# Kernel tuning notes

Hardware: AMD Instinct MI355X
Metric: run time of the kernel (lower is better)

Reference implementation:

```python
import jax, jax.numpy as jnp
import numpy as np

B, M, PAST, FUT, NPRED, D = 512, 32768, 8, 12, 20, 48


def _gru_step(h, x, w_ih, w_hh, b_ih, b_hh):
    # torch GRU cell: gates ordered [r, z, n]
    gi = x @ w_ih.T + b_ih
    gh = h @ w_hh.T + b_hh
    ir, iz, inn = jnp.split(gi, 3, axis=-1)
    hr, hz, hn = jnp.split(gh, 3, axis=-1)
    r = jax.nn.sigmoid(ir + hr)
    z = jax.nn.sigmoid(iz + hz)
    n = jnp.tanh(inn + r * hn)
    return (1.0 - z) * n + z * h


def setup_inputs() -> dict:
    key = jax.random.key(0)
    ks = jax.random.split(key, 16)
    f32 = jnp.float32
    def rn(k, shp, sc):
        return (jax.random.normal(k, shp, dtype=f32) * sc)
    return {
        "past": jax.random.normal(ks[0], (B, PAST, 2), dtype=f32),
        "obs_traj": jax.random.normal(ks[1], (B, PAST, 2), dtype=f32),
        "conv_w": rn(ks[2], (D, 2, 3), 0.3),
        "conv_b": jnp.zeros((D,), f32),
        "enc_w_ih": rn(ks[3], (3 * D, D), 0.1),
        "enc_w_hh": rn(ks[4], (3 * D, D), 0.1),
        "enc_b_ih": jnp.zeros((3 * D,), f32),
        "enc_b_hh": jnp.zeros((3 * D,), f32),
        "memory_past": jax.random.normal(ks[5], (M, D), dtype=f32),
        "memory_fut": jax.random.normal(ks[6], (M, D), dtype=f32),
        "Wq": rn(ks[7], (D, D), 0.1), "bq": jnp.zeros((D,), f32),
        "Wk": rn(ks[8], (D, D), 0.1), "bk": jnp.zeros((D,), f32),
        "Wv": rn(ks[9], (D, D), 0.1), "bv": jnp.zeros((D,), f32),
        "dec_w_ih": rn(ks[10], (6 * D, 2 * D), 0.1),
        "dec_w_hh": rn(ks[11], (6 * D, 2 * D), 0.1),
        "dec_b_ih": jnp.zeros((6 * D,), f32),
        "dec_b_hh": jnp.zeros((6 * D,), f32),
        "fc_w": rn(ks[12], (2, 2 * D), 0.1),
        "fc_b": jnp.zeros((2,), f32),
    }


def reference(past, obs_traj, conv_w, conv_b, enc_w_ih, enc_w_hh, enc_b_ih, enc_b_hh,
              memory_past, memory_fut, Wq, bq, Wk, bk, Wv, bv,
              dec_w_ih, dec_w_hh, dec_b_ih, dec_b_hh, fc_w, fc_b):
    b = past.shape[0]
    # --- past encoder: Conv1d(2,48,3,pad=1) + ReLU, then GRU(48,48) ---
    x = jnp.transpose(past, (0, 2, 1))                     # [B,2,T]
    emb = jax.lax.conv_general_dilated(
        x, conv_w, (1,), [(1, 1)], dimension_numbers=("NCH", "OIH", "NCH"))
    emb = jax.nn.relu(emb + conv_b[None, :, None])         # [B,48,T]
    emb = jnp.transpose(emb, (2, 0, 1))                    # [T,B,48] for scan

    def enc_step(h, x_t):
        return _gru_step(h, x_t, enc_w_ih, enc_w_hh, enc_b_ih, enc_b_hh), None
    state_past, _ = jax.lax.scan(enc_step, jnp.zeros((b, D), past.dtype), emb)  # [B,48]

    # --- iterative refinement: 20 rounds of attention over the full memory ---
    # Lin_K/Lin_V are applied to the same (full) banks every iteration -> hoist.
    K = memory_past @ Wk.T + bk                            # [M,48]
    V = memory_fut @ Wv.T + bv                             # [M,48]

    def irm_step(c, _):
        q = c @ Wq.T + bq                                  # [B,48]
        a = jax.nn.softmax(q @ K.T, axis=-1)               # [B,M], scale=1.0
        att = a @ V                                        # [B,48]
        return q + att, att
    _, atts = jax.lax.scan(irm_step, state_past, None, length=NPRED)  # [20,B,48]
    pred = jnp.transpose(atts, (1, 0, 2)).reshape(-1, D)   # [B*20,48] (b-major)

    # --- GRU(96,96) decoder, future_len steps, input only at t=0 ---
    n = b * NPRED
    present = jnp.repeat(obs_traj[:, -1], NPRED, axis=0)   # [B*20,2]
    sp = jnp.repeat(state_past, NPRED, axis=0)             # [B*20,48]
    info = jnp.concatenate([sp, pred], axis=1)             # [B*20,96]
    xs = jnp.concatenate(
        [info[None], jnp.zeros((FUT - 1, n, 2 * D), info.dtype)], axis=0)

    def dec_step(carry, x_t):
        h, pres = carry
        h = _gru_step(h, x_t, dec_w_ih, dec_w_hh, dec_b_ih, dec_b_hh)
        pres = pres + (h @ fc_w.T + fc_b)
        return (h, pres), pres
    _, coords = jax.lax.scan(
        dec_step, (jnp.zeros((n, 2 * D), info.dtype), present), xs)  # [FUT,B*20,2]

    prediction = jnp.transpose(coords, (1, 0, 2)).reshape(b, NPRED, FUT, 2)
    return prediction
```

## Files before the change

### kernel.cpp

```cpp
#include <hip/hip_runtime.h>

typedef unsigned short u16;
typedef unsigned int u32;
typedef __attribute__((ext_vector_type(8))) short short8v;
typedef __attribute__((ext_vector_type(4))) float f32x4;

#define GLD_LDS(g, l) __builtin_amdgcn_global_load_lds( \
    (const __attribute__((address_space(1))) void*)(g), \
    (__attribute__((address_space(3))) void*)(l), 16, 0, 0)

#define LOG2E 1.44269504f

__device__ __forceinline__ u16 f2bf(float f){
  union { float f; u32 u; } v; v.f = f;
  u32 r = v.u + 0x7FFFu + ((v.u >> 16) & 1u);
  return (u16)(r >> 16);
}
__device__ __forceinline__ float bf2f(u16 h){
  union { u32 u; float f; } v; v.u = ((u32)h) << 16;
  return v.f;
}
__device__ __forceinline__ u32 pk2(float a, float b){
  union { float f; u32 u; } x, y; x.f = a; y.f = b;
  return __builtin_amdgcn_perm(y.u + 0x8000u, x.u + 0x8000u, 0x07060302u);
}
__device__ __forceinline__ float sigm(float x){ return 1.f/(1.f+__expf(-x)); }
__device__ __forceinline__ float tanh_fast(float x){ return 1.f - 2.f/(1.f+__expf(2.f*x)); }

__global__ void prep_kernel(const float* dih, const float* dhh,
    const float* eih, const float* ehh, const float* wq, const float* wk, const float* wv,
    u16* Dih, u16* Dhh, u16* Eih, u16* Ehh, u16* Qf, u16* Kf, u16* Vf)
{
  int idx = blockIdx.x*256 + threadIdx.x;
  const float* src; u16* dst; int KC, Kc, e;
  if      (idx < 27648){ src=dih; dst=Dih; KC=3; Kc=96; e=idx; }
  else if (idx < 55296){ src=dhh; dst=Dhh; KC=3; Kc=96; e=idx-27648; }
  else if (idx < 64512){ src=eih; dst=Eih; KC=2; Kc=48; e=idx-55296; }
  else if (idx < 73728){ src=ehh; dst=Ehh; KC=2; Kc=48; e=idx-64512; }
  else if (idx < 76800){ src=wq;  dst=Qf;  KC=2; Kc=48; e=idx-73728; }
  else if (idx < 79872){ src=wk;  dst=Kf;  KC=2; Kc=48; e=idx-76800; }
  else if (idx < 82944){ src=wv;  dst=Vf;  KC=2; Kc=48; e=idx-79872; }
  else return;
  int j = e & 7, ln = (e>>3) & 15, qd = (e>>7) & 3, tkc = e>>9;
  int kc = tkc % KC, nt = tkc / KC;
  int g = nt*16 + ln, k = kc*32 + qd*8 + j;
  dst[e] = (k < Kc) ? f2bf(src[g*Kc + k]) : (u16)0;
}

__global__ __launch_bounds__(256) void setup_kernel(
    const float* past, const float* conv_w, const float* conv_b,
    const float* enc_b_ih, const float* enc_b_hh,
    const float* memory_past, const float* memory_fut,
    const float* bq, const float* bk, const float* bv,
    const u16* EihF, const u16* EhhF, const u16* WqF, const u16* WkF, const u16* WvF,
    float* stateP, float* qf, u16* qbB, u16* Kb, u16* Vc)
{
  __shared__ __align__(16) char SMEM[61440];
  const int tid = threadIdx.x, bx = blockIdx.x;
  const int wid = tid>>6, lane = tid&63, qd = lane>>4, ln = lane&15;
  f32x4 zf = {0.f,0.f,0.f,0.f};

  if (bx >= 504){
    int eb = bx - 504;
    u16* sWih = (u16*)(SMEM);
    u16* sWhh = (u16*)(SMEM + 18432);
    u16* sWq  = (u16*)(SMEM + 36864);
    float* sCw = (float*)(SMEM + 43008);
    float* sCb = (float*)(SMEM + 44160);
    float* sPast = (float*)(SMEM + 44352);
    u16* sHbW = (u16*)(SMEM + 48448 + wid*2304);
    for (int i = wid; i < 18; i += 4) GLD_LDS((const char*)EihF + i*1024 + lane*16, SMEM + i*1024);
    for (int i = wid; i < 18; i += 4) GLD_LDS((const char*)EhhF + i*1024 + lane*16, SMEM + 18432 + i*1024);
    for (int i = wid; i < 6;  i += 4) GLD_LDS((const char*)WqF  + i*1024 + lane*16, SMEM + 36864 + i*1024);
    for (int i = tid; i < 288; i += 256) sCw[i] = conv_w[i];
    if (tid < 48) sCb[tid] = conv_b[tid];
    for (int i = tid; i < 1024; i += 256) sPast[i] = past[eb*1024 + i];
    __syncthreads();
    short8v aE[8][2];
    {
      const float* pr = &sPast[(wid*16 + ln)*16];
      for (int t = 0; t < 8; ++t)
        for (int kc = 0; kc < 2; ++kc){
          union { short8v v; u16 h[8]; } u;
          #pragma unroll
          for (int j = 0; j < 8; ++j){
            int d = kc*32 + qd*8 + j;
            float a = 0.f;
            if (d < 48){
              a = sCb[d];
              #pragma unroll
              for (int kt = 0; kt < 3; ++kt){
                int tau = t + kt - 1;
                if (tau >= 0 && tau < 8){
                  a += pr[tau*2+0]*sCw[d*6+kt];
                  a += pr[tau*2+1]*sCw[d*6+3+kt];
                }
              }
              a = fmaxf(a, 0.f);
            }
            u.h[j] = (d < 48) ? f2bf(a) : (u16)0;
          }
          aE[t][kc] = u.v;
        }
    }
    for (int i = lane; i < 576; i += 64) ((u32*)sHbW)[i] = 0;
    float biR[3],biZ[3],biN[3],bhR[3],bhZ[3],bhN[3];
    #pragma unroll
    for (int i = 0; i < 3; ++i){
      int d = i*16 + ln;
      biR[i]=enc_b_ih[d]; biZ[i]=enc_b_ih[48+d]; biN[i]=enc_b_ih[96+d];
      bhR[i]=enc_b_hh[d]; bhZ[i]=enc_b_hh[48+d]; bhN[i]=enc_b_hh[96+d];
    }
    float hreg[3][4];
    #pragma unroll
    for (int i=0;i<3;++i) for (int r=0;r<4;++r) hreg[i][r]=0.f;
    int r0 = eb*64 + wid*16;
    #pragma unroll 1
    for (int t = 0; t < 8; ++t){
      short8v aH0 = *(const short8v*)&sHbW[ln*72 + qd*8];
      short8v aH1 = *(const short8v*)&sHbW[ln*72 + 32 + qd*8];
      f32x4 gI[9], gH[9];
      #pragma unroll
      for (int nt = 0; nt < 9; ++nt){ gI[nt] = zf; gH[nt] = zf; }
      #pragma unroll
      for (int nt = 0; nt < 9; ++nt){
        gI[nt] = __builtin_amdgcn_mfma_f32_16x16x32_bf16(aE[t][0], *(const short8v*)&sWih[((nt*2+0)*4+qd)*128 + ln*8], gI[nt], 0,0,0);
        gI[nt] = __builtin_amdgcn_mfma_f32_16x16x32_bf16(aE[t][1], *(const short8v*)&sWih[((nt*2+1)*4+qd)*128 + ln*8], gI[nt], 0,0,0);
        gH[nt] = __builtin_amdgcn_mfma_f32_16x16x32_bf16(aH0, *(const short8v*)&sWhh[((nt*2+0)*4+qd)*128 + ln*8], gH[nt], 0,0,0);
        gH[nt] = __builtin_amdgcn_mfma_f32_16x16x32_bf16(aH1, *(const short8v*)&sWhh[((nt*2+1)*4+qd)*128 + ln*8], gH[nt], 0,0,0);
      }
      #pragma unroll
      for (int i3 = 0; i3 < 3; ++i3)
        #pragma unroll
        for (int r = 0; r < 4; ++r){
          float rr = sigm(gI[i3][r]+biR[i3] + gH[i3][r]+bhR[i3]);
          float zz = sigm(gI[i3+3][r]+biZ[i3] + gH[i3+3][r]+bhZ[i3]);
          float nn = tanh_fast(gI[i3+6][r]+biN[i3] + rr*(gH[i3+6][r]+bhN[i3]));
          float hv = (1.f-zz)*nn + zz*hreg[i3][r];
          hreg[i3][r] = hv;
          sHbW[(qd*4+r)*72 + i3*16 + ln] = f2bf(hv);
        }
    }
    #pragma unroll
    for (int i3 = 0; i3 < 3; ++i3)
      #pragma unroll
      for (int r = 0; r < 4; ++r)
        stateP[(r0+qd*4+r)*48 + i3*16 + ln] = hreg[i3][r];
    short8v aH0 = *(const short8v*)&sHbW[ln*72 + qd*8];
    short8v aH1 = *(const short8v*)&sHbW[ln*72 + 32 + qd*8];
    f32x4 q3[3];
    #pragma unroll
    for (int nt = 0; nt < 3; ++nt){
      q3[nt] = zf;
      q3[nt] = __builtin_amdgcn_mfma_f32_16x16x32_bf16(aH0, *(const short8v*)&sWq[((nt*2+0)*4+qd)*128 + ln*8], q3[nt], 0,0,0);
      q3[nt] = __builtin_amdgcn_mfma_f32_16x16x32_bf16(aH1, *(const short8v*)&sWq[((nt*2+1)*4+qd)*128 + ln*8], q3[nt], 0,0,0);
    }
    #pragma unroll
    for (int nt = 0; nt < 3; ++nt)
      #pragma unroll
      for (int r = 0; r < 4; ++r){
        int row = r0 + qd*4 + r, d = nt*16 + ln;
        float v = q3[nt][r] + bq[d];
        qf[row*48 + d] = v;
        qbB[row*64 + d] = f2bf(v * LOG2E);
      }
    #pragma unroll
    for (int r = 0; r < 4; ++r)
      if (ln < 8) *(u32*)&qbB[(r0+qd*4+r)*64 + 48 + ln*2] = 0;
  } else {
    u16* sWkF = (u16*)(SMEM);
    u16* sWvF = (u16*)(SMEM + 6144);
    u16* smp  = (u16*)(SMEM + 12288 + wid*2304);
    u16* smf  = (u16*)(SMEM + 21504 + wid*2304);
    u16* sKT  = (u16*)(SMEM + 30720);
    u16* sVT  = (u16*)(SMEM + 38912);
    for (int i = wid; i < 6; i += 4) GLD_LDS((const char*)WkF + i*1024 + lane*16, SMEM + i*1024);
    for (int i = wid; i < 6; i += 4) GLD_LDS((const char*)WvF + i*1024 + lane*16, SMEM + 6144 + i*1024);
    float bkv[3], bvv[3];
    #pragma unroll
    for (int nt = 0; nt < 3; ++nt){ bkv[nt] = bk[nt*16+ln]; bvv[nt] = bv[nt*16+ln]; }
    int ntile = (bx < 8) ? 2 : 1;
    for (int tt = 0; tt < ntile; ++tt){
      int tile = (tt == 0) ? bx : (504 + bx);
      int r0 = tile*64 + wid*16;
      for (int i = lane; i < 576; i += 64){ ((u32*)smp)[i] = 0; ((u32*)smf)[i] = 0; }
      for (int i = lane; i < 768; i += 64){
        int r = i/48, c = i - r*48;
        smp[r*72+c] = f2bf(memory_past[(size_t)r0*48 + i]);
        smf[r*72+c] = f2bf(memory_fut[(size_t)r0*48 + i]);
      }
      __syncthreads();
      short8v aP0 = *(const short8v*)&smp[ln*72 + qd*8];
      short8v aP1 = *(const short8v*)&smp[ln*72 + 32 + qd*8];
      short8v aF0 = *(const short8v*)&smf[ln*72 + qd*8];
      short8v aF1 = *(const short8v*)&smf[ln*72 + 32 + qd*8];
      f32x4 k3[3], v3[3];
      #pragma unroll
      for (int nt = 0; nt < 3; ++nt){ k3[nt] = zf; v3[nt] = zf; }
      #pragma unroll
      for (int nt = 0; nt < 3; ++nt){
        k3[nt] = __builtin_amdgcn_mfma_f32_16x16x32_bf16(aP0, *(const short8v*)&sWkF[((nt*2+0)*4+qd)*128 + ln*8], k3[nt], 0,0,0);
        k3[nt] = __builtin_amdgcn_mfma_f32_16x16x32_bf16(aP1, *(const short8v*)&sWkF[((nt*2+1)*4+qd)*128 + ln*8], k3[nt], 0,0,0);
        v3[nt] = __builtin_amdgcn_mfma_f32_16x16x32_bf16(aF0, *(const short8v*)&sWvF[((nt*2+0)*4+qd)*128 + ln*8], v3[nt], 0,0,0);
        v3[nt] = __builtin_amdgcn_mfma_f32_16x16x32_bf16(aF1, *(const short8v*)&sWvF[((nt*2+1)*4+qd)*128 + ln*8], v3[nt], 0,0,0);
      }
      for (int i = lane; i < 128; i += 64) ((u32*)sKT)[(wid*16 + (i>>3))*32 + 24 + (i&7)] = 0;
      #pragma unroll
      for (int nt = 0; nt < 3; ++nt)
        #pragma unroll
        for (int r = 0; r < 4; ++r){
          int keyl = wid*16 + qd*4 + r, d = nt*16 + ln;
          sKT[keyl*64 + d] = f2bf(k3[nt][r] + bkv[nt]);
          sVT[d*72 + keyl] = f2bf(v3[nt][r] + bvv[nt]);
        }
      __syncthreads();
      for (int i = tid; i < 512; i += 256)
        *(uint4*)((char*)(Kb + (size_t)tile*64*64) + i*16) = *(const uint4*)((char*)sKT + i*16);
      for (int i = tid; i < 384; i += 256){
        int d = i>>3, sub = i&7;
        *(uint4*)((char*)(Vc + ((size_t)((tile*64)>>8)*48 + d)*256 + ((tile*64)&255)) + sub*16)
            = *(const uint4*)((char*)sVT + d*144 + sub*16);
      }
      __syncthreads();
    }
  }
}

__global__ __launch_bounds__(256, 1) void iter_kernel(int mode, int it,
    const u16* qbB, const u16* Kb, const u16* Vc, const u16* WqF, const float* bq,
    const float* qfP, float* qfC, float* pred,
    const float* mP, const float* lP, const float* aP,
    float* mC, float* lC, float* aC)
{
  __shared__ __align__(16) char SMEM[55936];
  u16*   sQ  = (u16*)(SMEM + 45056);
  float* sWc = (float*)(SMEM + 49152);
  float* sLg = (float*)(SMEM + 51200);
  u16*   sCb = (u16*)(SMEM + 51332);
  const int tid = threadIdx.x, bx = blockIdx.x;
  const int wid = tid>>6, lane = tid&63, qd = lane>>4, ln = lane&15;
  const int rg = bx>>4, ch = bx&15;
  const int rowbase = rg*32;
  f32x4 zf = {0.f,0.f,0.f,0.f};

  if (mode == 1){
    float* sRed = (float*)SMEM;
    {
      int row = tid>>3, jj = tid&7, grow = rowbase + row;
      float m0 = mP[grow*16 + jj*2], m1 = mP[grow*16 + jj*2+1];
      float l0 = lP[grow*16 + jj*2], l1 = lP[grow*16 + jj*2+1];
      float mg = fmaxf(m0, m1);
      #pragma unroll
      for (int k = 1; k < 8; k <<= 1) mg = fmaxf(mg, __shfl_xor(mg, k));
      float w0 = exp2f(m0 - mg), w1 = exp2f(m1 - mg);
      float wl = w0*l0 + w1*l1;
      #pragma unroll
      for (int k = 1; k < 8; k <<= 1) wl += __shfl_xor(wl, k);
      sWc[row*16 + jj*2] = w0; sWc[row*16 + jj*2+1] = w1;
      if (jj == 0) sLg[row] = wl;
    }
    __syncthreads();
    {
      f32x4 accv[6];
      #pragma unroll
      for (int i = 0; i < 6; ++i) accv[i] = zf;
      #pragma unroll
      for (int ci = 0; ci < 4; ++ci){
        int c = wid*4 + ci;
        const f32x4* slab = (const f32x4*)(aP + ((size_t)c*512 + rowbase)*48);
        #pragma unroll
        for (int i = 0; i < 6; ++i){
          f32x4 v = slab[i*64 + lane];
          int rr = (i*64 + lane)/12;
          float w = sWc[rr*16 + c];
          accv[i][0] += w*v[0]; accv[i][1] += w*v[1];
          accv[i][2] += w*v[2]; accv[i][3] += w*v[3];
        }
      }
      float* red = sRed + wid*1536;
      #pragma unroll
      for (int i = 0; i < 6; ++i)
        *(f32x4*)&red[(i*64 + lane)*4] = accv[i];
    }
    __syncthreads();
    {
      int row = tid>>3, jj = tid&7, grow = rowbase + row;
      float lg = sLg[row];
      int base = row*48 + jj*6;
      #pragma unroll
      for (int d6 = 0; d6 < 6; ++d6){
        int d = jj*6 + d6;
        float s = sRed[base+d6] + sRed[1536+base+d6] + sRed[3072+base+d6] + sRed[4608+base+d6];
        float a = s / lg;
        if (ch == 0) pred[(size_t)(grow*20 + (it-1))*48 + d] = a;
        sCb[row*72 + d] = f2bf(qfP[grow*48 + d] + a);
      }
      ((u32*)&sCb[row*72 + 48])[jj] = 0;
    }
    __syncthreads();
    if (wid < 2){
      short8v ac0 = *(const short8v*)&sCb[(wid*16+ln)*72 + qd*8];
      short8v ac1 = *(const short8v*)&sCb[(wid*16+ln)*72 + 32 + qd*8];
      f32x4 q3[3];
      #pragma unroll
      for (int nt = 0; nt < 3; ++nt){
        q3[nt] = zf;
        q3[nt] = __builtin_amdgcn_mfma_f32_16x16x32_bf16(ac0, *(const short8v*)&WqF[((nt*2+0)*4+qd)*128 + ln*8], q3[nt], 0,0,0);
        q3[nt] = __builtin_amdgcn_mfma_f32_16x16x32_bf16(ac1, *(const short8v*)&WqF[((nt*2+1)*4+qd)*128 + ln*8], q3[nt], 0,0,0);
      }
      #pragma unroll
      for (int nt = 0; nt < 3; ++nt)
        #pragma unroll
        for (int r = 0; r < 4; ++r){
          int lr = wid*16 + qd*4 + r, d = nt*16 + ln;
          float v = q3[nt][r] + bq[d];
          if (ch == 0) qfC[(rowbase + lr)*48 + d] = v;
          sQ[lr*64 + d] = f2bf(v * LOG2E);
        }
    } else {
      for (int i = tid-128; i < 256; i += 128){
        int r2 = i>>3, p = i&7;
        ((u32*)&sQ[r2*64 + 48])[p] = 0;
      }
    }
    __syncthreads();
  } else {
    const u32* src = (const u32*)(qbB + rowbase*64);
    ((u32*)sQ)[tid]       = src[tid];
    ((u32*)sQ)[256 + tid] = src[256 + tid];
    ((u32*)sQ)[512 + tid] = src[512 + tid];
    ((u32*)sQ)[768 + tid] = src[768 + tid];
    __syncthreads();
  }

  const int wslice = ch*2048 + wid*512;
  u16* sp8 = (u16*)(SMEM + 26624);
  short8v aq[2][2];
  #pragma unroll
  for (int rt = 0; rt < 2; ++rt)
    #pragma unroll
    for (int kc = 0; kc < 2; ++kc)
      aq[rt][kc] = *(const short8v*)&sQ[(rt*16+ln)*64 + kc*32 + qd*8];
  f32x4 acc[2][3];
  #pragma unroll
  for (int rt = 0; rt < 2; ++rt) for (int dt = 0; dt < 3; ++dt) acc[rt][dt] = zf;
  float mrun[2] = {-3.0e38f, -3.0e38f}, lrun[2] = {0.f, 0.f};
  u16* spb[2] = { sp8 + (wid*2+0)*1152, sp8 + (wid*2+1)*1152 };

  #pragma unroll
  for (int kt = 0; kt < 8; ++kt){
    const int tb = wslice + kt*64;
    const u16* kb = Kb + (size_t)tb*64;
    const u16* vb = Vc + (size_t)(tb>>8)*48*256 + (tb & 255);
    short8v kf[4][2], vf[2][3];
    #pragma unroll
    for (int nt = 0; nt < 4; ++nt)
      #pragma unroll
      for (int kc = 0; kc < 2; ++kc)
        kf[nt][kc] = *(const short8v*)&kb[(nt*16+ln)*64 + kc*32 + qd*8];
    #pragma unroll
    for (int kc = 0; kc < 2; ++kc)
      #pragma unroll
      for (int dt = 0; dt < 3; ++dt)
        vf[kc][dt] = *(const short8v*)&vb[(dt*16+ln)*256 + kc*32 + qd*8];
    f32x4 s[2][4];
    #pragma unroll
    for (int rt = 0; rt < 2; ++rt)
      #pragma unroll
      for (int nt = 0; nt < 4; ++nt){
        f32x4 z = zf;
        z = __builtin_amdgcn_mfma_f32_16x16x32_bf16(kf[nt][0], aq[rt][0], z, 0,0,0);
        z = __builtin_amdgcn_mfma_f32_16x16x32_bf16(kf[nt][1], aq[rt][1], z, 0,0,0);
        s[rt][nt] = z;
      }
    #pragma unroll
    for (int rt = 0; rt < 2; ++rt){
      float vmax = fmaxf(fmaxf(fmaxf(s[rt][0][0], s[rt][0][1]), fmaxf(s[rt][0][2], s[rt][0][3])),
                   fmaxf(fmaxf(s[rt][1][0], s[rt][1][1]), fmaxf(s[rt][1][2], s[rt][1][3])));
      vmax = fmaxf(vmax, fmaxf(fmaxf(fmaxf(s[rt][2][0], s[rt][2][1]), fmaxf(s[rt][2][2], s[rt][2][3])),
                   fmaxf(fmaxf(s[rt][3][0], s[rt][3][1]), fmaxf(s[rt][3][2], s[rt][3][3]))));
      vmax = fmaxf(vmax, __shfl_xor(vmax, 16));
      vmax = fmaxf(vmax, __shfl_xor(vmax, 32));
      float mnew = fmaxf(mrun[rt], vmax);
      float alpha = exp2f(mrun[rt] - mnew);
      mrun[rt] = mnew;
      u16* sp = spb[rt];
      float lsum = 0.f;
      #pragma unroll
      for (int nt = 0; nt < 4; ++nt){
        float p0 = exp2f(s[rt][nt][0]-mnew), p1 = exp2f(s[rt][nt][1]-mnew);
        float p2 = exp2f(s[rt][nt][2]-mnew), p3 = exp2f(s[rt][nt][3]-mnew);
        lsum += (p0+p1)+(p2+p3);
        uint2 pk; pk.x = pk2(p0,p1); pk.y = pk2(p2,p3);
        *(uint2*)&sp[ln*72 + nt*16 + qd*4] = pk;
      }
      lsum += __shfl_xor(lsum, 16);
      lsum += __shfl_xor(lsum, 32);
      lrun[rt] = lrun[rt]*alpha + lsum;
      #pragma unroll
      for (int dt = 0; dt < 3; ++dt){
        acc[rt][dt][0] *= alpha; acc[rt][dt][1] *= alpha;
        acc[rt][dt][2] *= alpha; acc[rt][dt][3] *= alpha;
      }
      short8v pb0 = *(const short8v*)&sp[ln*72 + qd*8];
      short8v pb1 = *(const short8v*)&sp[ln*72 + 32 + qd*8];
      #pragma unroll
      for (int dt = 0; dt < 3; ++dt){
        acc[rt][dt] = __builtin_amdgcn_mfma_f32_16x16x32_bf16(vf[0][dt], pb0, acc[rt][dt], 0,0,0);
        acc[rt][dt] = __builtin_amdgcn_mfma_f32_16x16x32_bf16(vf[1][dt], pb1, acc[rt][dt], 0,0,0);
      }
    }
  }
  __syncthreads();
  float* sMg = (float*)SMEM;
  #pragma unroll
  for (int rt = 0; rt < 2; ++rt)
    #pragma unroll
    for (int dt = 0; dt < 3; ++dt)
      #pragma unroll
      for (int r = 0; r < 4; ++r)
        sMg[wid*1600 + (rt*16+ln)*50 + dt*16 + qd*4 + r] = acc[rt][dt][r];
  if (lane < 16){
    sMg[wid*1600 + ln*50 + 48] = mrun[0]; sMg[wid*1600 + ln*50 + 49] = lrun[0];
    sMg[wid*1600 + (16+ln)*50 + 48] = mrun[1]; sMg[wid*1600 + (16+ln)*50 + 49] = lrun[1];
  }
  __syncthreads();
  {
    int row = tid>>3, jj = tid&7, grow = rowbase + row;
    float m0 = sMg[row*50+48], m1 = sMg[1600+row*50+48];
    float m2 = sMg[3200+row*50+48], m3 = sMg[4800+row*50+48];
    float mg = fmaxf(fmaxf(m0,m1), fmaxf(m2,m3));
    float e0 = exp2f(m0-mg), e1 = exp2f(m1-mg), e2 = exp2f(m2-mg), e3 = exp2f(m3-mg);
    float lg = e0*sMg[row*50+49] + e1*sMg[1600+row*50+49]
             + e2*sMg[3200+row*50+49] + e3*sMg[4800+row*50+49];
    if (jj == 0){ mC[grow*16 + ch] = mg; lC[grow*16 + ch] = lg; }
    int d0 = jj*6;
    #pragma unroll
    for (int d6 = 0; d6 < 6; ++d6){
      int d = d0 + d6;
      aC[((size_t)ch*512 + grow)*48 + d] =
          e0*sMg[row*50+d] + e1*sMg[1600+row*50+d]
        + e2*sMg[3200+row*50+d] + e3*sMg[4800+row*50+d];
    }
  }
}

__global__ __launch_bounds__(384, 1) void dec_kernel(
    const u16* Dihf, const u16* Dhhf, const float* b_ih, const float* b_hh,
    const float* stateP, const float* pred, const float* obs,
    const float* mF, const float* lF, const float* aF,
    const float* fc_w, const float* fc_b, float* out)
{
  __shared__ __align__(16) u16 sx[2][16*106];
  __shared__ float sPx[2][6][16], sPy[2][6][16];
  const int tid = threadIdx.x, bx = blockIdx.x;
  const int wid = tid>>6, lane = tid&63, qd = lane>>4, ln = lane&15;
  const int rw = bx*16;
  f32x4 zf = {0.f,0.f,0.f,0.f};

  for (int i = tid; i < 1536; i += 384){
    int r = i/96, k = i - r*96;
    int row = rw + r, b20 = row/20;
    float v = (k < 48) ? stateP[b20*48 + k] : pred[(size_t)row*48 + (k-48)];
    sx[0][r*106 + k] = f2bf(v);
  }
  if (tid < 48){
    int r19 = (19 - (rw % 20)) % 20;
    if (r19 < 16){
      int b = (rw + r19)/20;
      float mg = -3.0e38f, mv[16];
      #pragma unroll
      for (int c = 0; c < 16; ++c){ mv[c] = mF[b*16 + c]; mg = fmaxf(mg, mv[c]); }
      float num = 0.f, den = 0.f;
      #pragma unroll
      for (int c = 0; c < 16; ++c){
        float w = exp2f(mv[c] - mg);
        den += w * lF[b*16 + c];
        num += w * aF[((size_t)c*512 + b)*48 + tid];
      }
      sx[0][r19*106 + 48 + tid] = f2bf(num/den);
    }
  }
  short8v whh[3][3];
  #pragma unroll
  for (int g = 0; g < 3; ++g)
    #pragma unroll
    for (int kc = 0; kc < 3; ++kc)
      whh[g][kc] = *(const short8v*)&Dhhf[(((g*6+wid)*3+kc)*4+qd)*128 + ln*8];
  const int d = wid*16 + ln;
  float biR=b_ih[d], biZ=b_ih[96+d], biN=b_ih[192+d];
  float bhR=b_hh[d], bhZ=b_hh[96+d], bhN=b_hh[192+d];
  float fw0=fc_w[d], fw1=fc_w[96+d];
  float hold[4] = {0.f,0.f,0.f,0.f};
  float fcb0 = fc_b[0], fcb1 = fc_b[1];
  float pres0 = 0.f, pres1 = 0.f;
  if (wid == 0 && lane < 16){
    int b20 = (rw + lane)/20;
    pres0 = obs[b20*16 + 14];
    pres1 = obs[b20*16 + 15];
  }
  __syncthreads();

  #pragma unroll 1
  for (int t = 0; t < 12; ++t){
    const u16* sr = sx[t&1];
    u16* sw = sx[(t+1)&1];
    short8v xa0 = *(const short8v*)&sr[ln*106 + qd*8];
    short8v xa1 = *(const short8v*)&sr[ln*106 + 32 + qd*8];
    short8v xa2 = *(const short8v*)&sr[ln*106 + 64 + qd*8];
    f32x4 acc[3] = {zf, zf, zf};
    if (t == 0){
      #pragma unroll
      for (int g = 0; g < 3; ++g){
        int nt = g*6 + wid;
        acc[g] = __builtin_amdgcn_mfma_f32_16x16x32_bf16(xa0, *(const short8v*)&Dihf[((nt*3+0)*4+qd)*128 + ln*8], acc[g], 0,0,0);
        acc[g] = __builtin_amdgcn_mfma_f32_16x16x32_bf16(xa1, *(const short8v*)&Dihf[((nt*3+1)*4+qd)*128 + ln*8], acc[g], 0,0,0);
        acc[g] = __builtin_amdgcn_mfma_f32_16x16x32_bf16(xa2, *(const short8v*)&Dihf[((nt*3+2)*4+qd)*128 + ln*8], acc[g], 0,0,0);
      }
    } else {
      #pragma unroll
      for (int g = 0; g < 3; ++g){
        acc[g] = __builtin_amdgcn_mfma_f32_16x16x32_bf16(xa0, whh[g][0], acc[g], 0,0,0);
        acc[g] = __builtin_amdgcn_mfma_f32_16x16x32_bf16(xa1, whh[g][1], acc[g], 0,0,0);
        acc[g] = __builtin_amdgcn_mfma_f32_16x16x32_bf16(xa2, whh[g][2], acc[g], 0,0,0);
      }
    }
    float px[4], py[4];
    #pragma unroll
    for (int r = 0; r < 4; ++r){
      float rr = sigm(acc[0][r] + biR + bhR);
      float zz = sigm(acc[1][r] + biZ + bhZ);
      float nn = (t == 0) ? tanh_fast(acc[2][r] + biN + rr*bhN)
                          : tanh_fast(biN + rr*(acc[2][r] + bhN));
      float hv = (1.f-zz)*nn + zz*hold[r];
      hold[r] = hv;
      sw[(qd*4+r)*106 + d] = f2bf(hv);
      px[r] = fw0*hv;
      py[r] = fw1*hv;
    }
    #pragma unroll
    for (int msk = 8; msk >= 1; msk >>= 1)
      #pragma unroll
      for (int r = 0; r < 4; ++r){
        px[r] += __shfl_xor(px[r], msk);
        py[r] += __shfl_xor(py[r], msk);
      }
    if (ln == 0){
      #pragma unroll
      for (int r = 0; r < 4; ++r){
        sPx[t&1][wid][qd*4+r] = px[r];
        sPy[t&1][wid][qd*4+r] = py[r];
      }
    }
    __syncthreads();
    if (wid == 0 && lane < 16){
      float fx = 0.f, fy = 0.f;
      #pragma unroll
      for (int w = 0; w < 6; ++w){ fx += sPx[t&1][w][lane]; fy += sPy[t&1][w][lane]; }
      pres0 += fx + fcb0;
      pres1 += fy + fcb1;
      out[((size_t)(rw + lane)*12 + t)*2 + 0] = pres0;
      out[((size_t)(rw + lane)*12 + t)*2 + 1] = pres1;
    }
  }
}

extern "C" void kernel_launch(void* const* d_in, const int* in_sizes, int n_in,
                              void* d_out, int out_size, void* d_ws, size_t ws_size,
                              hipStream_t stream)
{
  const float* past        = (const float*)d_in[0];
  const float* obs         = (const float*)d_in[1];
  const float* conv_w      = (const float*)d_in[2];
  const float* conv_b      = (const float*)d_in[3];
  const float* enc_w_ih    = (const float*)d_in[4];
  const float* enc_w_hh    = (const float*)d_in[5];
  const float* enc_b_ih    = (const float*)d_in[6];
  const float* enc_b_hh    = (const float*)d_in[7];
  const float* memory_past = (const float*)d_in[8];
  const float* memory_fut  = (const float*)d_in[9];
  const float* Wq = (const float*)d_in[10];
  const float* bq = (const float*)d_in[11];
  const float* Wk = (const float*)d_in[12];
  const float* bk = (const float*)d_in[13];
  const float* Wv = (const float*)d_in[14];
  const float* bv = (const float*)d_in[15];
  const float* dec_w_ih = (const float*)d_in[16];
  const float* dec_w_hh = (const float*)d_in[17];
  const float* dec_b_ih = (const float*)d_in[18];
  const float* dec_b_hh = (const float*)d_in[19];
  const float* fc_w = (const float*)d_in[20];
  const float* fc_b = (const float*)d_in[21];
  float* out = (float*)d_out;

  char* ws = (char*)d_ws;
  size_t off = 0;
  auto alloc = [&](size_t bytes){ void* p = ws + off; off += (bytes + 255) & ~(size_t)255; return p; };
  float* stateP = (float*)alloc(512*48*4);
  float* qfA    = (float*)alloc(512*48*4);
  float* qfB    = (float*)alloc(512*48*4);
  u16*   qbB    = (u16*)alloc(512*64*2);
  float* mB[2], *lB[2], *aB[2];
  for (int i = 0; i < 2; ++i){
    mB[i] = (float*)alloc(512*16*4);
    lB[i] = (float*)alloc(512*16*4);
    aB[i] = (float*)alloc((size_t)512*16*48*4);
  }
  float* pred = (float*)alloc((size_t)10240*48*4);
  u16*   Kb   = (u16*)alloc((size_t)32768*64*2);
  u16*   Vc   = (u16*)alloc((size_t)32768*48*2);
  u16*   Dihf = (u16*)alloc(27648*2);
  u16*   Dhhf = (u16*)alloc(27648*2);
  u16*   EihF = (u16*)alloc(9216*2);
  u16*   EhhF = (u16*)alloc(9216*2);
  u16*   WqF  = (u16*)alloc(3072*2);
  u16*   WkF  = (u16*)alloc(3072*2);
  u16*   WvF  = (u16*)alloc(3072*2);
  float* qbuf[2] = { qfA, qfB };

  prep_kernel<<<324, 256, 0, stream>>>(dec_w_ih, dec_w_hh, enc_w_ih, enc_w_hh,
                                       Wq, Wk, Wv, Dihf, Dhhf, EihF, EhhF, WqF, WkF, WvF);

  setup_kernel<<<512, 256, 0, stream>>>(
      past, conv_w, conv_b, enc_b_ih, enc_b_hh, memory_past, memory_fut,
      bq, bk, bv, EihF, EhhF, WqF, WkF, WvF,
      stateP, qfA, qbB, Kb, Vc);

  iter_kernel<<<256, 256, 0, stream>>>(0, 0, qbB, Kb, Vc, WqF, bq,
      qfA, qfA, pred, mB[1], lB[1], aB[1], mB[0], lB[0], aB[0]);
  for (int it = 1; it < 20; ++it){
    int pv = (it-1)&1, cu = it&1;
    iter_kernel<<<256, 256, 0, stream>>>(1, it, qbB, Kb, Vc, WqF, bq,
        qbuf[pv], qbuf[cu], pred, mB[pv], lB[pv], aB[pv], mB[cu], lB[cu], aB[cu]);
  }

  dec_kernel<<<640, 384, 0, stream>>>(Dihf, Dhhf, dec_b_ih, dec_b_hh,
      stateP, pred, obs, mB[1], lB[1], aB[1], fc_w, fc_b, out);
}
```

Baseline: 628.7 us.

## Spread encoder GRU over more blocks, store partial attention in bf16, tweak decoder stride

Result: faster. 584.2 us (-7.1%).

```diff
diff --git a/kernel.cpp b/kernel.cpp
--- a/kernel.cpp
+++ b/kernel.cpp
@@ -19,6 +19,12 @@
 __device__ __forceinline__ float bf2f(u16 h){
   union { u32 u; float f; } v; v.u = ((u32)h) << 16;
   return v.f;
+}
+__device__ __forceinline__ float bflo(u32 x){
+  union { u32 u; float f; } v; v.u = x << 16; return v.f;
+}
+__device__ __forceinline__ float bfhi(u32 x){
+  union { u32 u; float f; } v; v.u = x & 0xFFFF0000u; return v.f;
 }
 __device__ __forceinline__ u32 pk2(float a, float b){
   union { float f; u32 u; } x, y; x.f = a; y.f = b;
@@ -60,26 +66,29 @@
   const int wid = tid>>6, lane = tid&63, qd = lane>>4, ln = lane&15;
   f32x4 zf = {0.f,0.f,0.f,0.f};
 
-  if (bx >= 504){
-    int eb = bx - 504;
-    u16* sWih = (u16*)(SMEM);
-    u16* sWhh = (u16*)(SMEM + 18432);
-    u16* sWq  = (u16*)(SMEM + 36864);
-    float* sCw = (float*)(SMEM + 43008);
-    float* sCb = (float*)(SMEM + 44160);
-    float* sPast = (float*)(SMEM + 44352);
-    u16* sHbW = (u16*)(SMEM + 48448 + wid*2304);
-    for (int i = wid; i < 18; i += 4) GLD_LDS((const char*)EihF + i*1024 + lane*16, SMEM + i*1024);
-    for (int i = wid; i < 18; i += 4) GLD_LDS((const char*)EhhF + i*1024 + lane*16, SMEM + 18432 + i*1024);
-    for (int i = wid; i < 6;  i += 4) GLD_LDS((const char*)WqF  + i*1024 + lane*16, SMEM + 36864 + i*1024);
+  if (bx >= 480){
+    const int eb = bx - 480;
+    const int r0 = eb*16;
+    u16*   sWf  = (u16*)(SMEM);
+    u16*   gIb  = (u16*)(SMEM + 18432);
+    u16*   sHb0 = (u16*)(SMEM + 55296);
+    u16*   sHb1 = (u16*)(SMEM + 57600);
+    float* sCw  = (float*)(SMEM + 57600);
+    float* sCb  = (float*)(SMEM + 58752);
+    float* sPast= (float*)(SMEM + 58944);
+
+    for (int i = wid; i < 18; i += 4) GLD_LDS((const char*)EihF + i*1024 + lane*16, (char*)sWf + i*1024);
     for (int i = tid; i < 288; i += 256) sCw[i] = conv_w[i];
     if (tid < 48) sCb[tid] = conv_b[tid];
-    for (int i = tid; i < 1024; i += 256) sPast[i] = past[eb*1024 + i];
-    __syncthreads();
-    short8v aE[8][2];
-    {
-      const float* pr = &sPast[(wid*16 + ln)*16];
-      for (int t = 0; t < 8; ++t)
+    for (int i = tid; i < 256; i += 256) sPast[i] = past[r0*16 + i];
+    __syncthreads();
+    #pragma unroll
+    for (int tt = 0; tt < 2; ++tt){
+      int t = wid*2 + tt;
+      short8v aE[2];
+      {
+        const float* pr = &sPast[ln*16];
+        #pragma unroll
         for (int kc = 0; kc < 2; ++kc){
           union { short8v v; u16 h[8]; } u;
           #pragma unroll
@@ -100,73 +109,93 @@
             }
             u.h[j] = (d < 48) ? f2bf(a) : (u16)0;
           }
-          aE[t][kc] = u.v;
+          aE[kc] = u.v;
         }
-    }
-    for (int i = lane; i < 576; i += 64) ((u32*)sHbW)[i] = 0;
-    float biR[3],biZ[3],biN[3],bhR[3],bhZ[3],bhN[3];
-    #pragma unroll
-    for (int i = 0; i < 3; ++i){
-      int d = i*16 + ln;
-      biR[i]=enc_b_ih[d]; biZ[i]=enc_b_ih[48+d]; biN[i]=enc_b_ih[96+d];
-      bhR[i]=enc_b_hh[d]; bhZ[i]=enc_b_hh[48+d]; bhN[i]=enc_b_hh[96+d];
-    }
-    float hreg[3][4];
-    #pragma unroll
-    for (int i=0;i<3;++i) for (int r=0;r<4;++r) hreg[i][r]=0.f;
-    int r0 = eb*64 + wid*16;
+      }
+      f32x4 gI[9];
+      #pragma unroll
+      for (int nt = 0; nt < 9; ++nt) gI[nt] = zf;
+      #pragma unroll
+      for (int nt = 0; nt < 9; ++nt){
+        gI[nt] = __builtin_amdgcn_mfma_f32_16x16x32_bf16(aE[0], *(const short8v*)&sWf[((nt*2+0)*4+qd)*128 + ln*8], gI[nt], 0,0,0);
+        gI[nt] = __builtin_amdgcn_mfma_f32_16x16x32_bf16(aE[1], *(const short8v*)&sWf[((nt*2+1)*4+qd)*128 + ln*8], gI[nt], 0,0,0);
+      }
+      #pragma unroll
+      for (int nt = 0; nt < 9; ++nt)
+        #pragma unroll
+        for (int r = 0; r < 4; ++r)
+          gIb[t*2304 + (qd*4+r)*144 + nt*16 + ln] = f2bf(gI[nt][r]);
+    }
+    __syncthreads();
+    for (int i = wid; i < 18; i += 4) GLD_LDS((const char*)EhhF + i*1024 + lane*16, (char*)sWf + i*1024);
+    for (int i = tid; i < 1152; i += 256) ((u32*)sHb0)[i] = 0;
+    __syncthreads();
+
+    const int g = wid;
+    float biR=0, biZ=0, biN=0, bhR=0, bhZ=0, bhN=0;
+    if (g < 3){
+      int d = g*16 + ln;
+      biR = enc_b_ih[d]; biZ = enc_b_ih[48+d]; biN = enc_b_ih[96+d];
+      bhR = enc_b_hh[d]; bhZ = enc_b_hh[48+d]; bhN = enc_b_hh[96+d];
+    }
+    float hold[4] = {0.f,0.f,0.f,0.f};
     #pragma unroll 1
     for (int t = 0; t < 8; ++t){
-      short8v aH0 = *(const short8v*)&sHbW[ln*72 + qd*8];
-      short8v aH1 = *(const short8v*)&sHbW[ln*72 + 32 + qd*8];
-      f32x4 gI[9], gH[9];
-      #pragma unroll
-      for (int nt = 0; nt < 9; ++nt){ gI[nt] = zf; gH[nt] = zf; }
-      #pragma unroll
-      for (int nt = 0; nt < 9; ++nt){
-        gI[nt] = __builtin_amdgcn_mfma_f32_16x16x32_bf16(aE[t][0], *(const short8v*)&sWih[((nt*2+0)*4+qd)*128 + ln*8], gI[nt], 0,0,0);
-        gI[nt] = __builtin_amdgcn_mfma_f32_16x16x32_bf16(aE[t][1], *(const short8v*)&sWih[((nt*2+1)*4+qd)*128 + ln*8], gI[nt], 0,0,0);
-        gH[nt] = __builtin_amdgcn_mfma_f32_16x16x32_bf16(aH0, *(const short8v*)&sWhh[((nt*2+0)*4+qd)*128 + ln*8], gH[nt], 0,0,0);
-        gH[nt] = __builtin_amdgcn_mfma_f32_16x16x32_bf16(aH1, *(const short8v*)&sWhh[((nt*2+1)*4+qd)*128 + ln*8], gH[nt], 0,0,0);
-      }
-      #pragma unroll
-      for (int i3 = 0; i3 < 3; ++i3)
+      u16* sr = (t & 1) ? sHb1 : sHb0;
+      u16* sw = (t & 1) ? sHb0 : sHb1;
+      if (g < 3){
+        short8v aH0 = *(const short8v*)&sr[ln*72 + qd*8];
+        short8v aH1 = *(const short8v*)&sr[ln*72 + 32 + qd*8];
+        f32x4 aR = zf, aZ = zf, aN = zf;
+        aR = __builtin_amdgcn_mfma_f32_16x16x32_bf16(aH0, *(const short8v*)&sWf[(((g  )*2+0)*4+qd)*128 + ln*8], aR, 0,0,0);
+        aR = __builtin_amdgcn_mfma_f32_16x16x32_bf16(aH1, *(const short8v*)&sWf[(((g  )*2+1)*4+qd)*128 + ln*8], aR, 0,0,0);
+        aZ = __builtin_amdgcn_mfma_f32_16x16x32_bf16(aH0, *(const short8v*)&sWf[(((3+g)*2+0)*4+qd)*128 + ln*8], aZ, 0,0,0);
+        aZ = __builtin_amdgcn_mfma_f32_16x16x32_bf16(aH1, *(const short8v*)&sWf[(((3+g)*2+1)*4+qd)*128 + ln*8], aZ, 0,0,0);
+        aN = __builtin_amdgcn_mfma_f32_16x16x32_bf16(aH0, *(const short8v*)&sWf[(((6+g)*2+0)*4+qd)*128 + ln*8], aN, 0,0,0);
+        aN = __builtin_amdgcn_mfma_f32_16x16x32_bf16(aH1, *(const short8v*)&sWf[(((6+g)*2+1)*4+qd)*128 + ln*8], aN, 0,0,0);
         #pragma unroll
         for (int r = 0; r < 4; ++r){
-          float rr = sigm(gI[i3][r]+biR[i3] + gH[i3][r]+bhR[i3]);
-          float zz = sigm(gI[i3+3][r]+biZ[i3] + gH[i3+3][r]+bhZ[i3]);
-          float nn = tanh_fast(gI[i3+6][r]+biN[i3] + rr*(gH[i3+6][r]+bhN[i3]));
-          float hv = (1.f-zz)*nn + zz*hreg[i3][r];
-          hreg[i3][r] = hv;
-          sHbW[(qd*4+r)*72 + i3*16 + ln] = f2bf(hv);
+          int row = qd*4 + r;
+          float giR = bf2f(gIb[t*2304 + row*144 +      g*16 + ln]);
+          float giZ = bf2f(gIb[t*2304 + row*144 + 48 + g*16 + ln]);
+          float giN = bf2f(gIb[t*2304 + row*144 + 96 + g*16 + ln]);
+          float rr = sigm(giR + biR + aR[r] + bhR);
+          float zz = sigm(giZ + biZ + aZ[r] + bhZ);
+          float nn = tanh_fast(giN + biN + rr*(aN[r] + bhN));
+          float hv = (1.f-zz)*nn + zz*hold[r];
+          hold[r] = hv;
+          sw[row*72 + g*16 + ln] = f2bf(hv);
         }
-    }
-    #pragma unroll
-    for (int i3 = 0; i3 < 3; ++i3)
+      }
+      __syncthreads();
+    }
+    if (g < 3)
       #pragma unroll
       for (int r = 0; r < 4; ++r)
-        stateP[(r0+qd*4+r)*48 + i3*16 + ln] = hreg[i3][r];
-    short8v aH0 = *(const short8v*)&sHbW[ln*72 + qd*8];
-    short8v aH1 = *(const short8v*)&sHbW[ln*72 + 32 + qd*8];
-    f32x4 q3[3];
-    #pragma unroll
-    for (int nt = 0; nt < 3; ++nt){
-      q3[nt] = zf;
-      q3[nt] = __builtin_amdgcn_mfma_f32_16x16x32_bf16(aH0, *(const short8v*)&sWq[((nt*2+0)*4+qd)*128 + ln*8], q3[nt], 0,0,0);
-      q3[nt] = __builtin_amdgcn_mfma_f32_16x16x32_bf16(aH1, *(const short8v*)&sWq[((nt*2+1)*4+qd)*128 + ln*8], q3[nt], 0,0,0);
-    }
-    #pragma unroll
-    for (int nt = 0; nt < 3; ++nt)
-      #pragma unroll
-      for (int r = 0; r < 4; ++r){
-        int row = r0 + qd*4 + r, d = nt*16 + ln;
-        float v = q3[nt][r] + bq[d];
-        qf[row*48 + d] = v;
-        qbB[row*64 + d] = f2bf(v * LOG2E);
-      }
-    #pragma unroll
-    for (int r = 0; r < 4; ++r)
-      if (ln < 8) *(u32*)&qbB[(r0+qd*4+r)*64 + 48 + ln*2] = 0;
+        stateP[(r0 + qd*4 + r)*48 + g*16 + ln] = hold[r];
+    if (wid == 0){
+      short8v aH0 = *(const short8v*)&sHb0[ln*72 + qd*8];
+      short8v aH1 = *(const short8v*)&sHb0[ln*72 + 32 + qd*8];
+      f32x4 q3[3];
+      #pragma unroll
+      for (int nt = 0; nt < 3; ++nt){
+        q3[nt] = zf;
+        q3[nt] = __builtin_amdgcn_mfma_f32_16x16x32_bf16(aH0, *(const short8v*)&WqF[((nt*2+0)*4+qd)*128 + ln*8], q3[nt], 0,0,0);
+        q3[nt] = __builtin_amdgcn_mfma_f32_16x16x32_bf16(aH1, *(const short8v*)&WqF[((nt*2+1)*4+qd)*128 + ln*8], q3[nt], 0,0,0);
+      }
+      #pragma unroll
+      for (int nt = 0; nt < 3; ++nt)
+        #pragma unroll
+        for (int r = 0; r < 4; ++r){
+          int row = r0 + qd*4 + r, d = nt*16 + ln;
+          float v = q3[nt][r] + bq[d];
+          qf[row*48 + d] = v;
+          qbB[row*64 + d] = f2bf(v * LOG2E);
+        }
+      #pragma unroll
+      for (int r = 0; r < 4; ++r)
+        if (ln < 8) *(u32*)&qbB[(r0+qd*4+r)*64 + 48 + ln*2] = 0;
+    }
   } else {
     u16* sWkF = (u16*)(SMEM);
     u16* sWvF = (u16*)(SMEM + 6144);
@@ -179,9 +208,9 @@
     float bkv[3], bvv[3];
     #pragma unroll
     for (int nt = 0; nt < 3; ++nt){ bkv[nt] = bk[nt*16+ln]; bvv[nt] = bv[nt*16+ln]; }
-    int ntile = (bx < 8) ? 2 : 1;
+    int ntile = (bx < 32) ? 2 : 1;
     for (int tt = 0; tt < ntile; ++tt){
-      int tile = (tt == 0) ? bx : (504 + bx);
+      int tile = (tt == 0) ? bx : (480 + bx);
       int r0 = tile*64 + wid*16;
       for (int i = lane; i < 576; i += 64){ ((u32*)smp)[i] = 0; ((u32*)smf)[i] = 0; }
       for (int i = lane; i < 768; i += 64){
@@ -229,8 +258,8 @@
 __global__ __launch_bounds__(256, 1) void iter_kernel(int mode, int it,
     const u16* qbB, const u16* Kb, const u16* Vc, const u16* WqF, const float* bq,
     const float* qfP, float* qfC, float* pred,
-    const float* mP, const float* lP, const float* aP,
-    float* mC, float* lC, float* aC)
+    const float* mP, const float* lP, const u16* aP,
+    float* mC, float* lC, u16* aC)
 {
   __shared__ __align__(16) char SMEM[55936];
   u16*   sQ  = (u16*)(SMEM + 45056);
@@ -267,14 +296,15 @@
       #pragma unroll
       for (int ci = 0; ci < 4; ++ci){
         int c = wid*4 + ci;
-        const f32x4* slab = (const f32x4*)(aP + ((size_t)c*512 + rowbase)*48);
+        const u16* slab = aP + ((size_t)c*512 + rowbase)*48;
         #pragma unroll
         for (int i = 0; i < 6; ++i){
-          f32x4 v = slab[i*64 + lane];
-          int rr = (i*64 + lane)/12;
+          int idx = i*64 + lane;
+          uint2 u = *(const uint2*)&slab[idx*4];
+          int rr = idx/12;
           float w = sWc[rr*16 + c];
-          accv[i][0] += w*v[0]; accv[i][1] += w*v[1];
-          accv[i][2] += w*v[2]; accv[i][3] += w*v[3];
+          accv[i][0] += w*bflo(u.x); accv[i][1] += w*bfhi(u.x);
+          accv[i][2] += w*bflo(u.y); accv[i][3] += w*bfhi(u.y);
         }
       }
       float* red = sRed + wid*1536;
@@ -435,23 +465,27 @@
              + e2*sMg[3200+row*50+49] + e3*sMg[4800+row*50+49];
     if (jj == 0){ mC[grow*16 + ch] = mg; lC[grow*16 + ch] = lg; }
     int d0 = jj*6;
+    float sv[6];
     #pragma unroll
     for (int d6 = 0; d6 < 6; ++d6){
       int d = d0 + d6;
-      aC[((size_t)ch*512 + grow)*48 + d] =
-          e0*sMg[row*50+d] + e1*sMg[1600+row*50+d]
-        + e2*sMg[3200+row*50+d] + e3*sMg[4800+row*50+d];
-    }
-  }
-}
-
-__global__ __launch_bounds__(384, 1) void dec_kernel(
+      sv[d6] = e0*sMg[row*50+d] + e1*sMg[1600+row*50+d]
+             + e2*sMg[3200+row*50+d] + e3*sMg[4800+row*50+d];
+    }
+    u16* ac = aC + ((size_t)ch*512 + grow)*48 + d0;
+    *(u32*)&ac[0] = pk2(sv[0], sv[1]);
+    *(u32*)&ac[2] = pk2(sv[2], sv[3]);
+    *(u32*)&ac[4] = pk2(sv[4], sv[5]);
+  }
+}
+
+__global__ __launch_bounds__(384) void dec_kernel(
     const u16* Dihf, const u16* Dhhf, const float* b_ih, const float* b_hh,
     const float* stateP, const float* pred, const float* obs,
-    const float* mF, const float* lF, const float* aF,
+    const float* mF, const float* lF, const u16* aF,
     const float* fc_w, const float* fc_b, float* out)
 {
-  __shared__ __align__(16) u16 sx[2][16*106];
+  __shared__ __align__(16) u16 sx[2][16*104];
   __shared__ float sPx[2][6][16], sPy[2][6][16];
   const int tid = threadIdx.x, bx = blockIdx.x;
   const int wid = tid>>6, lane = tid&63, qd = lane>>4, ln = lane&15;
@@ -462,7 +496,7 @@
     int r = i/96, k = i - r*96;
     int row = rw + r, b20 = row/20;
     float v = (k < 48) ? stateP[b20*48 + k] : pred[(size_t)row*48 + (k-48)];
-    sx[0][r*106 + k] = f2bf(v);
+    sx[0][r*104 + k] = f2bf(v);
   }
   if (tid < 48){
     int r19 = (19 - (rw % 20)) % 20;
@@ -476,9 +510,9 @@
       for (int c = 0; c < 16; ++c){
         float w = exp2f(mv[c] - mg);
         den += w * lF[b*16 + c];
-        num += w * aF[((size_t)c*512 + b)*48 + tid];
-      }
-      sx[0][r19*106 + 48 + tid] = f2bf(num/den);
+        num += w * bf2f(aF[((size_t)c*512 + b)*48 + tid]);
+      }
+      sx[0][r19*104 + 48 + tid] = f2bf(num/den);
     }
   }
   short8v whh[3][3];
@@ -505,9 +539,9 @@
   for (int t = 0; t < 12; ++t){
     const u16* sr = sx[t&1];
     u16* sw = sx[(t+1)&1];
-    short8v xa0 = *(const short8v*)&sr[ln*106 + qd*8];
-    short8v xa1 = *(const short8v*)&sr[ln*106 + 32 + qd*8];
-    short8v xa2 = *(const short8v*)&sr[ln*106 + 64 + qd*8];
+    short8v xa0 = *(const short8v*)&sr[ln*104 + qd*8];
+    short8v xa1 = *(const short8v*)&sr[ln*104 + 32 + qd*8];
+    short8v xa2 = *(const short8v*)&sr[ln*104 + 64 + qd*8];
     f32x4 acc[3] = {zf, zf, zf};
     if (t == 0){
       #pragma unroll
@@ -534,7 +568,7 @@
                           : tanh_fast(biN + rr*(acc[2][r] + bhN));
       float hv = (1.f-zz)*nn + zz*hold[r];
       hold[r] = hv;
-      sw[(qd*4+r)*106 + d] = f2bf(hv);
+      sw[(qd*4+r)*104 + d] = f2bf(hv);
       px[r] = fw0*hv;
       py[r] = fw1*hv;
     }
@@ -600,11 +634,12 @@
   float* qfA    = (float*)alloc(512*48*4);
   float* qfB    = (float*)alloc(512*48*4);
   u16*   qbB    = (u16*)alloc(512*64*2);
-  float* mB[2], *lB[2], *aB[2];
+  float* mB[2], *lB[2];
+  u16*   aB[2];
   for (int i = 0; i < 2; ++i){
     mB[i] = (float*)alloc(512*16*4);
     lB[i] = (float*)alloc(512*16*4);
-    aB[i] = (float*)alloc((size_t)512*16*48*4);
+    aB[i] = (u16*)alloc((size_t)512*16*48*2);
   }
   float* pred = (float*)alloc((size_t)10240*48*4);
   u16*   Kb   = (u16*)alloc((size_t)32768*64*2);
```
